# Kernel optimization log

Measured on AMD Instinct MI355X. Metric: run time of the kernel, lower is better.

## Reference

```python
import jax, jax.numpy as jnp
import numpy as np

SIGMA = 1e-4  # BlendParams().sigma default in pytorch3d


def setup_inputs() -> dict:
    key = jax.random.key(0)
    k1, k2, k3, k4 = jax.random.split(key, 4)
    N, H, W, K = 8, 512, 512, 16
    # z-buffer depths (positive in front of camera, arbitrary for background)
    zbuf = jax.random.uniform(k1, (N, H, W, K), jnp.float32, 0.1, 10.0)
    # signed 2D distances pixel-center -> face edge, on the scale of sigma
    dists = jax.random.normal(k2, (N, H, W, K), jnp.float32) * 1e-4
    p2f = jax.random.randint(k3, (N, H, W, K), 0, 20000)
    drop = jax.random.uniform(k4, (N, H, W, K)) < 0.2
    pix_to_face = jnp.where(drop, -1, p2f).astype(jnp.int64)
    return {"zbuf": zbuf, "dists": dists, "pix_to_face": pix_to_face}


def reference(zbuf, dists, pix_to_face):
    # colors = zbuf repeated over 3 channels; blend uses top face only for RGB
    # sigmoid_alpha_blend:
    #   prob  = sigmoid(-dists / sigma) * (pix_to_face >= 0)
    #   alpha = 1 - prod_K (1 - prob)
    #   rgb   = colors[..., 0, :]  (== zbuf[..., 0] broadcast to 3 channels)
    mask = (pix_to_face >= 0).astype(zbuf.dtype)  # [N,H,W,K]
    prob = jax.nn.sigmoid(-dists / SIGMA) * mask  # [N,H,W,K]
    alpha = 1.0 - jnp.prod(1.0 - prob, axis=-1)   # [N,H,W]
    rgb = jnp.broadcast_to(zbuf[..., 0:1], zbuf.shape[:-1] + (3,))  # [N,H,W,3]
    return jnp.concatenate([rgb, alpha[..., None]], axis=-1)  # [N,H,W,4]
```

## Files before the change

### kernel.cpp

```cpp
#include <hip/hip_runtime.h>

#define INV_SIGMA 1.0e4f
#define ROUNDS 8

typedef float v4f __attribute__((ext_vector_type(4)));
typedef int   v4i __attribute__((ext_vector_type(4)));

__device__ __forceinline__ float one_minus_prob(float d, int f) {
    float s = 1.0f / (1.0f + __expf(-d * INV_SIGMA));
    return (f >= 0) ? s : 1.0f;
}

__global__ __launch_bounds__(256) void SelfShader_9921374454199_kernel(
    const float* __restrict__ zbuf,
    const float* __restrict__ dists,
    const int*   __restrict__ p2f,
    float*       __restrict__ out,
    long long nChunks)
{
    const int t = threadIdx.x;
    const long long cbase = (long long)blockIdx.x * (256 * ROUNDS) + t;

    const v4f* d4 = reinterpret_cast<const v4f*>(dists);
    const v4i* f4 = reinterpret_cast<const v4i*>(p2f);

    if (cbase + (ROUNDS - 1) * 256 < nChunks) {
        v4f   d[ROUNDS];
        v4i   f[ROUNDS];
        float z[ROUNDS];
#pragma unroll
        for (int r = 0; r < ROUNDS; ++r) {
            long long c = cbase + r * 256;
            d[r] = __builtin_nontemporal_load(d4 + c);
            f[r] = __builtin_nontemporal_load(f4 + c);
            z[r] = __builtin_nontemporal_load(zbuf + ((c >> 2) << 4));
        }
#pragma unroll
        for (int r = 0; r < ROUNDS; ++r) {
            long long c = cbase + r * 256;
            float prod = one_minus_prob(d[r].x, f[r].x) * one_minus_prob(d[r].y, f[r].y)
                       * one_minus_prob(d[r].z, f[r].z) * one_minus_prob(d[r].w, f[r].w);
            prod *= __shfl_xor(prod, 1, 4);
            prod *= __shfl_xor(prod, 2, 4);
            float v = ((t & 3) == 3) ? (1.0f - prod) : z[r];
            __builtin_nontemporal_store(v, out + c);
        }
    } else {
        for (int r = 0; r < ROUNDS; ++r) {
            long long c = cbase + r * 256;
            if (c >= nChunks) break;
            v4f   dd = d4[c];
            v4i   ff = f4[c];
            float zz = zbuf[(c >> 2) << 4];
            float prod = one_minus_prob(dd.x, ff.x) * one_minus_prob(dd.y, ff.y)
                       * one_minus_prob(dd.z, ff.z) * one_minus_prob(dd.w, ff.w);
            prod *= __shfl_xor(prod, 1, 4);
            prod *= __shfl_xor(prod, 2, 4);
            out[c] = ((t & 3) == 3) ? (1.0f - prod) : zz;
        }
    }
}

extern "C" void kernel_launch(void* const* d_in, const int* in_sizes, int n_in,
                              void* d_out, int out_size, void* d_ws, size_t ws_size,
                              hipStream_t stream) {
    const float* zbuf  = (const float*)d_in[0];
    const float* dists = (const float*)d_in[1];
    const int*   p2f   = (const int*)d_in[2];
    float*       out   = (float*)d_out;

    long long nChunks = (long long)in_sizes[0] / 4;
    const long long chunksPerBlock = 256LL * ROUNDS;
    int grid = (int)((nChunks + chunksPerBlock - 1) / chunksPerBlock);
    SelfShader_9921374454199_kernel<<<grid, 256, 0, stream>>>(zbuf, dists, p2f, out, nChunks);
}
```

Measured before the change: 332.0 us.

## Issue loads via inline asm with staged vmcnt waits and smaller per-block tiles

Each block now covers 1024 chunks instead of 2048, and each wave owns a contiguous 256-chunk span. All twelve global loads (four rounds of dists, face ids and zbuf) are issued up front in inline assembly using immediate offsets. Explicit s_waitcnt vmcnt steps then let each round's compute and store start as soon as its own loads land, instead of waiting for all loads. This relies on hand-counted vmcnt values and sched barriers, which is fragile because stores also count toward vmcnt on this architecture. It also launches twice as many blocks.

```diff
diff --git a/kernel.cpp b/kernel.cpp
--- a/kernel.cpp
+++ b/kernel.cpp
@@ -1,7 +1,6 @@
 #include <hip/hip_runtime.h>
 
 #define INV_SIGMA 1.0e4f
-#define ROUNDS 8
 
 typedef float v4f __attribute__((ext_vector_type(4)));
 typedef int   v4i __attribute__((ext_vector_type(4)));
@@ -9,6 +8,12 @@
 __device__ __forceinline__ float one_minus_prob(float d, int f) {
     float s = 1.0f / (1.0f + __expf(-d * INV_SIGMA));
     return (f >= 0) ? s : 1.0f;
+}
+
+__device__ __forceinline__ float quad_combine(float prod) {
+    prod *= __shfl_xor(prod, 1, 4);
+    prod *= __shfl_xor(prod, 2, 4);
+    return prod;
 }
 
 __global__ __launch_bounds__(256) void SelfShader_9921374454199_kernel(
@@ -19,43 +24,88 @@
     long long nChunks)
 {
     const int t = threadIdx.x;
-    const long long cbase = (long long)blockIdx.x * (256 * ROUNDS) + t;
+    const long long blockBase = (long long)blockIdx.x * 1024;
 
-    const v4f* d4 = reinterpret_cast<const v4f*>(dists);
-    const v4i* f4 = reinterpret_cast<const v4i*>(p2f);
+    if (blockBase + 1024 <= nChunks) {
+        const int wave = t >> 6;
+        const int lane = t & 63;
+        const long long c0 = blockBase + (long long)wave * 256 + lane;
 
-    if (cbase + (ROUNDS - 1) * 256 < nChunks) {
-        v4f   d[ROUNDS];
-        v4i   f[ROUNDS];
-        float z[ROUNDS];
-#pragma unroll
-        for (int r = 0; r < ROUNDS; ++r) {
-            long long c = cbase + r * 256;
-            d[r] = __builtin_nontemporal_load(d4 + c);
-            f[r] = __builtin_nontemporal_load(f4 + c);
-            z[r] = __builtin_nontemporal_load(zbuf + ((c >> 2) << 4));
+        const float* dA = dists + (c0 << 2);
+        const int*   fA = p2f   + (c0 << 2);
+        const float* zA = zbuf  + ((c0 >> 2) << 4);
+
+        v4f d0, d1, d2, d3;
+        v4i f0, f1, f2, f3;
+        float z0, z1, z2, z3;
+
+        asm volatile(
+            "global_load_dwordx4 %0, %12, off\n\t"
+            "global_load_dwordx4 %4, %13, off\n\t"
+            "global_load_dword   %8, %14, off\n\t"
+            "global_load_dwordx4 %1, %12, off offset:1024\n\t"
+            "global_load_dwordx4 %5, %13, off offset:1024\n\t"
+            "global_load_dword   %9, %14, off offset:1024\n\t"
+            "global_load_dwordx4 %2, %12, off offset:2048\n\t"
+            "global_load_dwordx4 %6, %13, off offset:2048\n\t"
+            "global_load_dword   %10, %14, off offset:2048\n\t"
+            "global_load_dwordx4 %3, %12, off offset:3072\n\t"
+            "global_load_dwordx4 %7, %13, off offset:3072\n\t"
+            "global_load_dword   %11, %14, off offset:3072\n\t"
+            : "=&v"(d0), "=&v"(d1), "=&v"(d2), "=&v"(d3),
+              "=&v"(f0), "=&v"(f1), "=&v"(f2), "=&v"(f3),
+              "=&v"(z0), "=&v"(z1), "=&v"(z2), "=&v"(z3)
+            : "v"(dA), "v"(fA), "v"(zA)
+            : "memory");
+
+        const bool isAlpha = (t & 3) == 3;
+
+        asm volatile("s_waitcnt vmcnt(9)" ::: "memory");
+        __builtin_amdgcn_sched_barrier(0);
+        {
+            float p = one_minus_prob(d0.x, f0.x) * one_minus_prob(d0.y, f0.y)
+                    * one_minus_prob(d0.z, f0.z) * one_minus_prob(d0.w, f0.w);
+            p = quad_combine(p);
+            float v = isAlpha ? (1.0f - p) : z0;
+            __builtin_nontemporal_store(v, out + c0);
         }
-#pragma unroll
-        for (int r = 0; r < ROUNDS; ++r) {
-            long long c = cbase + r * 256;
-            float prod = one_minus_prob(d[r].x, f[r].x) * one_minus_prob(d[r].y, f[r].y)
-                       * one_minus_prob(d[r].z, f[r].z) * one_minus_prob(d[r].w, f[r].w);
-            prod *= __shfl_xor(prod, 1, 4);
-            prod *= __shfl_xor(prod, 2, 4);
-            float v = ((t & 3) == 3) ? (1.0f - prod) : z[r];
-            __builtin_nontemporal_store(v, out + c);
+        asm volatile("s_waitcnt vmcnt(7)" ::: "memory");
+        __builtin_amdgcn_sched_barrier(0);
+        {
+            float p = one_minus_prob(d1.x, f1.x) * one_minus_prob(d1.y, f1.y)
+                    * one_minus_prob(d1.z, f1.z) * one_minus_prob(d1.w, f1.w);
+            p = quad_combine(p);
+            float v = isAlpha ? (1.0f - p) : z1;
+            __builtin_nontemporal_store(v, out + c0 + 64);
+        }
+        asm volatile("s_waitcnt vmcnt(5)" ::: "memory");
+        __builtin_amdgcn_sched_barrier(0);
+        {
+            float p = one_minus_prob(d2.x, f2.x) * one_minus_prob(d2.y, f2.y)
+                    * one_minus_prob(d2.z, f2.z) * one_minus_prob(d2.w, f2.w);
+            p = quad_combine(p);
+            float v = isAlpha ? (1.0f - p) : z2;
+            __builtin_nontemporal_store(v, out + c0 + 128);
+        }
+        asm volatile("s_waitcnt vmcnt(3)" ::: "memory");
+        __builtin_amdgcn_sched_barrier(0);
+        {
+            float p = one_minus_prob(d3.x, f3.x) * one_minus_prob(d3.y, f3.y)
+                    * one_minus_prob(d3.z, f3.z) * one_minus_prob(d3.w, f3.w);
+            p = quad_combine(p);
+            float v = isAlpha ? (1.0f - p) : z3;
+            __builtin_nontemporal_store(v, out + c0 + 192);
         }
     } else {
-        for (int r = 0; r < ROUNDS; ++r) {
-            long long c = cbase + r * 256;
-            if (c >= nChunks) break;
+        const v4f* d4 = reinterpret_cast<const v4f*>(dists);
+        const v4i* f4 = reinterpret_cast<const v4i*>(p2f);
+        for (long long c = blockBase + t; c < nChunks; c += 256) {
             v4f   dd = d4[c];
             v4i   ff = f4[c];
             float zz = zbuf[(c >> 2) << 4];
             float prod = one_minus_prob(dd.x, ff.x) * one_minus_prob(dd.y, ff.y)
                        * one_minus_prob(dd.z, ff.z) * one_minus_prob(dd.w, ff.w);
-            prod *= __shfl_xor(prod, 1, 4);
-            prod *= __shfl_xor(prod, 2, 4);
+            prod = quad_combine(prod);
             out[c] = ((t & 3) == 3) ? (1.0f - prod) : zz;
         }
     }
@@ -70,7 +120,7 @@
     float*       out   = (float*)d_out;
 
     long long nChunks = (long long)in_sizes[0] / 4;
-    const long long chunksPerBlock = 256LL * ROUNDS;
+    const long long chunksPerBlock = 1024;
     int grid = (int)((nChunks + chunksPerBlock - 1) / chunksPerBlock);
     SelfShader_9921374454199_kernel<<<grid, 256, 0, stream>>>(zbuf, dists, p2f, out, nChunks);
 }
```

Result: slower. 359.8 us (+8.4%).

## Map one thread per pixel with vectorized float4 output store

Applied to the files above, without the earlier changes.

Replaces the four-lanes-per-pixel scheme with cross-lane shuffles and 8 unrolled rounds by a one-thread-per-pixel mapping. Each thread loads all 16 depth/face entries of its pixel with four 16-byte loads per array, reduces the product locally, and writes the RGBA output with a single vector store. This removes shuffles and the per-lane select and cuts store instructions. In exchange, each load instruction now accesses lanes 64 bytes apart rather than contiguously, and per-thread ILP from the unrolled rounds is gone.

```diff
diff --git a/kernel.cpp b/kernel.cpp
--- a/kernel.cpp
+++ b/kernel.cpp
@@ -1,7 +1,6 @@
 #include <hip/hip_runtime.h>
 
 #define INV_SIGMA 1.0e4f
-#define ROUNDS 8
 
 typedef float v4f __attribute__((ext_vector_type(4)));
 typedef int   v4i __attribute__((ext_vector_type(4)));
@@ -16,49 +15,41 @@
     const float* __restrict__ dists,
     const int*   __restrict__ p2f,
     float*       __restrict__ out,
-    long long nChunks)
+    long long nPixels)
 {
-    const int t = threadIdx.x;
-    const long long cbase = (long long)blockIdx.x * (256 * ROUNDS) + t;
+    const long long p = (long long)blockIdx.x * 256 + threadIdx.x;
+    if (p >= nPixels) return;
 
-    const v4f* d4 = reinterpret_cast<const v4f*>(dists);
-    const v4i* f4 = reinterpret_cast<const v4i*>(p2f);
+    const v4f* d4 = reinterpret_cast<const v4f*>(dists) + (p << 2);
+    const v4i* f4 = reinterpret_cast<const v4i*>(p2f)   + (p << 2);
 
-    if (cbase + (ROUNDS - 1) * 256 < nChunks) {
-        v4f   d[ROUNDS];
-        v4i   f[ROUNDS];
-        float z[ROUNDS];
-#pragma unroll
-        for (int r = 0; r < ROUNDS; ++r) {
-            long long c = cbase + r * 256;
-            d[r] = __builtin_nontemporal_load(d4 + c);
-            f[r] = __builtin_nontemporal_load(f4 + c);
-            z[r] = __builtin_nontemporal_load(zbuf + ((c >> 2) << 4));
-        }
-#pragma unroll
-        for (int r = 0; r < ROUNDS; ++r) {
-            long long c = cbase + r * 256;
-            float prod = one_minus_prob(d[r].x, f[r].x) * one_minus_prob(d[r].y, f[r].y)
-                       * one_minus_prob(d[r].z, f[r].z) * one_minus_prob(d[r].w, f[r].w);
-            prod *= __shfl_xor(prod, 1, 4);
-            prod *= __shfl_xor(prod, 2, 4);
-            float v = ((t & 3) == 3) ? (1.0f - prod) : z[r];
-            __builtin_nontemporal_store(v, out + c);
-        }
-    } else {
-        for (int r = 0; r < ROUNDS; ++r) {
-            long long c = cbase + r * 256;
-            if (c >= nChunks) break;
-            v4f   dd = d4[c];
-            v4i   ff = f4[c];
-            float zz = zbuf[(c >> 2) << 4];
-            float prod = one_minus_prob(dd.x, ff.x) * one_minus_prob(dd.y, ff.y)
-                       * one_minus_prob(dd.z, ff.z) * one_minus_prob(dd.w, ff.w);
-            prod *= __shfl_xor(prod, 1, 4);
-            prod *= __shfl_xor(prod, 2, 4);
-            out[c] = ((t & 3) == 3) ? (1.0f - prod) : zz;
-        }
-    }
+    v4f d0 = __builtin_nontemporal_load(d4 + 0);
+    v4f d1 = __builtin_nontemporal_load(d4 + 1);
+    v4f d2 = __builtin_nontemporal_load(d4 + 2);
+    v4f d3 = __builtin_nontemporal_load(d4 + 3);
+    v4i f0 = __builtin_nontemporal_load(f4 + 0);
+    v4i f1 = __builtin_nontemporal_load(f4 + 1);
+    v4i f2 = __builtin_nontemporal_load(f4 + 2);
+    v4i f3 = __builtin_nontemporal_load(f4 + 3);
+    float z = __builtin_nontemporal_load(zbuf + (p << 4));
+
+    float c0 = ((one_minus_prob(d0.x, f0.x) * one_minus_prob(d0.y, f0.y))
+               * one_minus_prob(d0.z, f0.z)) * one_minus_prob(d0.w, f0.w);
+    float c1 = ((one_minus_prob(d1.x, f1.x) * one_minus_prob(d1.y, f1.y))
+               * one_minus_prob(d1.z, f1.z)) * one_minus_prob(d1.w, f1.w);
+    float c2 = ((one_minus_prob(d2.x, f2.x) * one_minus_prob(d2.y, f2.y))
+               * one_minus_prob(d2.z, f2.z)) * one_minus_prob(d2.w, f2.w);
+    float c3 = ((one_minus_prob(d3.x, f3.x) * one_minus_prob(d3.y, f3.y))
+               * one_minus_prob(d3.z, f3.z)) * one_minus_prob(d3.w, f3.w);
+
+    float P = (c0 * c1) * (c2 * c3);
+
+    v4f o;
+    o.x = z;
+    o.y = z;
+    o.z = z;
+    o.w = 1.0f - P;
+    __builtin_nontemporal_store(o, reinterpret_cast<v4f*>(out) + p);
 }
 
 extern "C" void kernel_launch(void* const* d_in, const int* in_sizes, int n_in,
@@ -69,8 +60,7 @@
     const int*   p2f   = (const int*)d_in[2];
     float*       out   = (float*)d_out;
 
-    long long nChunks = (long long)in_sizes[0] / 4;
-    const long long chunksPerBlock = 256LL * ROUNDS;
-    int grid = (int)((nChunks + chunksPerBlock - 1) / chunksPerBlock);
-    SelfShader_9921374454199_kernel<<<grid, 256, 0, stream>>>(zbuf, dists, p2f, out, nChunks);
+    long long nPixels = (long long)in_sizes[0] / 16;
+    int grid = (int)((nPixels + 255) / 256);
+    SelfShader_9921374454199_kernel<<<grid, 256, 0, stream>>>(zbuf, dists, p2f, out, nPixels);
 }
```

Result: slower. 349.4 us (+5.2%).
